# Kernel tuning notes

Hardware: AMD Instinct MI355X
Metric: run time of the kernel (lower is better)

Reference implementation:

```python
import jax, jax.numpy as jnp
import numpy as np

B, F_G, F_L, F_INT = 2, 64, 64, 32
D = H = W = 64
BN_EPS = 1e-5


def setup_inputs() -> dict:
    key = jax.random.key(0)
    ks = jax.random.split(key, 8)
    g = jax.random.normal(ks[0], (B, F_G, D, H, W), dtype=jnp.float32)
    x = jax.random.normal(ks[1], (B, F_L, D, H, W), dtype=jnp.float32)
    # Gating MLP (1x1x1 convs on pooled features == dense layers)
    w1 = jax.random.normal(ks[2], (F_INT, F_G + F_L), dtype=jnp.float32) * (1.0 / np.sqrt(F_G + F_L))
    b1 = jnp.zeros((F_INT,), dtype=jnp.float32)
    w2 = jax.random.normal(ks[3], (F_G * F_L, F_INT), dtype=jnp.float32) * (1.0 / np.sqrt(F_INT))
    b2 = jnp.zeros((F_G * F_L,), dtype=jnp.float32)
    # psi: Conv3d(F_l, 1, k=1) + BatchNorm3d(1) (inference-mode stats)
    psi_w = jax.random.normal(ks[4], (F_L,), dtype=jnp.float32) * (1.0 / np.sqrt(F_L))
    psi_b = jnp.zeros((1,), dtype=jnp.float32)
    bn_gamma = jnp.ones((1,), dtype=jnp.float32)
    bn_beta = jnp.zeros((1,), dtype=jnp.float32)
    bn_mean = jnp.zeros((1,), dtype=jnp.float32)
    bn_var = jnp.ones((1,), dtype=jnp.float32)
    return {"g": g, "x": x, "w1": w1, "b1": b1, "w2": w2, "b2": b2,
            "psi_w": psi_w, "psi_b": psi_b, "bn_gamma": bn_gamma,
            "bn_beta": bn_beta, "bn_mean": bn_mean, "bn_var": bn_var}


def reference(g, x, w1, b1, w2, b2, psi_w, psi_b, bn_gamma, bn_beta, bn_mean, bn_var):
    # Global average pool of cat([g, x]) -> [B, F_g+F_l]
    pooled = jnp.concatenate([jnp.mean(g, axis=(2, 3, 4)), jnp.mean(x, axis=(2, 3, 4))], axis=1)
    h = jax.nn.relu(pooled @ w1.T + b1)                       # [B, F_int]
    dw = jax.nn.sigmoid(h @ w2.T + b2).reshape(B, F_G, F_L)   # dynamic weights [B, F_g, F_l]
    # attended[b,l,d,h,w] = sum_g g[b,g,d,h,w] * dw[b,g,l]  (batched GEMM, no 6D blow-up)
    attended = jnp.einsum('bgdhw,bgl->bldhw', g, dw)
    # psi: 1x1x1 conv to 1 channel + BN + sigmoid
    s = jnp.einsum('bldhw,l->bdhw', attended, psi_w) + psi_b[0]
    s = (s - bn_mean[0]) * (bn_gamma[0] / jnp.sqrt(bn_var[0] + BN_EPS)) + bn_beta[0]
    return x * jax.nn.sigmoid(s)[:, None]                     # [B, F_l, D, H, W]
```

## Files before the change

### kernel.cpp

```cpp
#include <hip/hip_runtime.h>
#include <math.h>

#define SPATIAL (64*64*64)
#define SPATIAL4 (SPATIAL/4)
#define OCT4  (SPATIAL4/8)
#define NCH 64
#define BN_EPS 1e-5f

typedef float v4f __attribute__((ext_vector_type(4)));

__global__ __launch_bounds__(256, 8) void mean_kernel(const float* __restrict__ g,
                                                      const float* __restrict__ x,
                                                      float* __restrict__ partial) {
    int blk = blockIdx.x;
    int ch  = blk >> 3;
    int oct = blk & 7;
    bool isg = ch < 128;
    const float* src = isg
        ? g + (size_t)ch * SPATIAL
        : x + (size_t)(ch - 128) * SPATIAL;
    const v4f* s4 = (const v4f*)src + (size_t)oct * OCT4 + threadIdx.x;

    float acc[8] = {0.f,0.f,0.f,0.f,0.f,0.f,0.f,0.f};
    if (isg) {
        for (int it = 0; it < 4; ++it) {
            #pragma unroll
            for (int j = 0; j < 8; ++j) {
                v4f v = __builtin_nontemporal_load(s4 + j * 256);
                acc[j] += (v.x + v.y) + (v.z + v.w);
            }
            s4 += 2048;
        }
    } else {
        for (int it = 0; it < 4; ++it) {
            #pragma unroll
            for (int j = 0; j < 8; ++j) {
                v4f v = s4[j * 256];
                acc[j] += (v.x + v.y) + (v.z + v.w);
            }
            s4 += 2048;
        }
    }
    float sum = ((acc[0] + acc[1]) + (acc[2] + acc[3]))
              + ((acc[4] + acc[5]) + (acc[6] + acc[7]));

    #pragma unroll
    for (int off = 32; off > 0; off >>= 1)
        sum += __shfl_down(sum, off, 64);
    __shared__ float wsum[4];
    int lane = threadIdx.x & 63, wave = threadIdx.x >> 6;
    if (lane == 0) wsum[wave] = sum;
    __syncthreads();
    if (threadIdx.x == 0)
        partial[blk] = wsum[0] + wsum[1] + wsum[2] + wsum[3];
}

__global__ __launch_bounds__(64) void mlp_kernel(const float* __restrict__ partial,
                           const float* __restrict__ w1, const float* __restrict__ b1,
                           const float* __restrict__ w2, const float* __restrict__ b2,
                           const float* __restrict__ psi_w, const float* __restrict__ psi_b,
                           const float* __restrict__ bn_gamma, const float* __restrict__ bn_beta,
                           const float* __restrict__ bn_mean, const float* __restrict__ bn_var,
                           float* __restrict__ coef) {
    __shared__ float p[256];
    __shared__ float h[32];
    int tid = threadIdx.x;
    int blk = blockIdx.x;
    int b = blk >> 6, gc = blk & 63;

    #pragma unroll
    for (int ch = tid; ch < 256; ch += 64) {
        const float* pp = partial + 8 * ch;
        float s = ((pp[0] + pp[1]) + (pp[2] + pp[3]))
                + ((pp[4] + pp[5]) + (pp[6] + pp[7]));
        int pi = (ch < 128) ? ((ch >> 6) * 128 + (ch & 63))
                            : (((ch - 128) >> 6) * 128 + 64 + ((ch - 128) & 63));
        p[pi] = s * (1.0f / SPATIAL);
    }
    __syncthreads();
    if (tid < 32) {
        float acc = b1[tid];
        const float* wr = w1 + tid * 128;
        #pragma unroll 4
        for (int k = 0; k < 128; ++k) acc += p[b * 128 + k] * wr[k];
        h[tid] = fmaxf(acc, 0.f);
    }
    __syncthreads();
    const float4* wr = (const float4*)(w2 + (size_t)(gc * 64 + tid) * 32);
    float z = b2[gc * 64 + tid];
    #pragma unroll
    for (int j = 0; j < 8; ++j) {
        float4 wv = wr[j];
        z += h[4*j] * wv.x + h[4*j+1] * wv.y + h[4*j+2] * wv.z + h[4*j+3] * wv.w;
    }
    float sig = 1.f / (1.f + expf(-z));
    float val = sig * psi_w[tid];
    #pragma unroll
    for (int off = 32; off > 0; off >>= 1)
        val += __shfl_down(val, off, 64);
    float scale = bn_gamma[0] * rsqrtf(bn_var[0] + BN_EPS);
    if (tid == 0) coef[b * 64 + gc] = val * scale;
    if (blk == 0 && tid == 0)
        coef[128] = (psi_b[0] - bn_mean[0]) * scale + bn_beta[0];
}

__device__ __forceinline__ void fma4(v4f& a, v4f v, float c) {
    a.x += v.x * c; a.y += v.y * c; a.z += v.z * c; a.w += v.w * c;
}

__global__ __launch_bounds__(256, 8) void apply_kernel(const float* __restrict__ g,
                                                       const float* __restrict__ x,
                                                       const float* __restrict__ coef,
                                                       float* __restrict__ out) {
    int t    = threadIdx.x;
    int pos  = t & 63;
    int grp  = t >> 6;
    int blk  = blockIdx.x;
    int batch = blk >> 10;
    int base4 = (blk & 1023) * 64 + pos;
    size_t bOff = (size_t)batch * NCH * SPATIAL4;

    const v4f* g4 = (const v4f*)g;
    const v4f* x4 = (const v4f*)x;
    v4f* o4 = (v4f*)out;

    const v4f* cfv = (const v4f*)(coef + batch * NCH + grp * 16);
    const v4f* gp = g4 + bOff + (size_t)(grp * 16) * SPATIAL4 + base4;

    v4f acc0 = {0.f,0.f,0.f,0.f}, acc1 = {0.f,0.f,0.f,0.f};
    #pragma unroll
    for (int bq = 0; bq < 4; ++bq) {
        v4f cv = cfv[bq];
        v4f v0 = __builtin_nontemporal_load(gp + (size_t)(4*bq + 0) * SPATIAL4);
        v4f v1 = __builtin_nontemporal_load(gp + (size_t)(4*bq + 1) * SPATIAL4);
        v4f v2 = __builtin_nontemporal_load(gp + (size_t)(4*bq + 2) * SPATIAL4);
        v4f v3 = __builtin_nontemporal_load(gp + (size_t)(4*bq + 3) * SPATIAL4);
        fma4(acc0, v0, cv.x);
        fma4(acc1, v1, cv.y);
        fma4(acc0, v2, cv.z);
        fma4(acc1, v3, cv.w);
    }
    v4f acc = {acc0.x + acc1.x, acc0.y + acc1.y, acc0.z + acc1.z, acc0.w + acc1.w};

    __shared__ v4f red[4][64];
    if (grp != 0) red[grp][pos] = acc;
    __syncthreads();
    if (grp == 0) {
        v4f r1 = red[1][pos], r2 = red[2][pos], r3 = red[3][pos];
        float d = coef[128];
        v4f s;
        s.x = 1.f / (1.f + expf(-(acc.x + r1.x + r2.x + r3.x + d)));
        s.y = 1.f / (1.f + expf(-(acc.y + r1.y + r2.y + r3.y + d)));
        s.z = 1.f / (1.f + expf(-(acc.z + r1.z + r2.z + r3.z + d)));
        s.w = 1.f / (1.f + expf(-(acc.w + r1.w + r2.w + r3.w + d)));
        red[0][pos] = s;
    }
    __syncthreads();
    v4f s = red[0][pos];

    const v4f* xp = x4 + bOff + (size_t)(grp * 16) * SPATIAL4 + base4;
    v4f*       op = o4 + bOff + (size_t)(grp * 16) * SPATIAL4 + base4;
    #pragma unroll 4
    for (int l = 0; l < 16; ++l) {
        v4f xv = xp[(size_t)l * SPATIAL4];
        v4f ov = {xv.x * s.x, xv.y * s.y, xv.z * s.z, xv.w * s.w};
        __builtin_nontemporal_store(ov, op + (size_t)l * SPATIAL4);
    }
}

extern "C" void kernel_launch(void* const* d_in, const int* in_sizes, int n_in,
                              void* d_out, int out_size, void* d_ws, size_t ws_size,
                              hipStream_t stream) {
    const float* g        = (const float*)d_in[0];
    const float* x        = (const float*)d_in[1];
    const float* w1       = (const float*)d_in[2];
    const float* b1       = (const float*)d_in[3];
    const float* w2       = (const float*)d_in[4];
    const float* b2       = (const float*)d_in[5];
    const float* psi_w    = (const float*)d_in[6];
    const float* psi_b    = (const float*)d_in[7];
    const float* bn_gamma = (const float*)d_in[8];
    const float* bn_beta  = (const float*)d_in[9];
    const float* bn_mean  = (const float*)d_in[10];
    const float* bn_var   = (const float*)d_in[11];
    float* out = (float*)d_out;
    float* ws  = (float*)d_ws;

    float* partial = ws;
    float* coef    = ws + 2048;

    mean_kernel<<<2048, 256, 0, stream>>>(g, x, partial);
    mlp_kernel<<<128, 64, 0, stream>>>(partial, w1, b1, w2, b2, psi_w, psi_b,
                                       bn_gamma, bn_beta, bn_mean, bn_var, coef);
    apply_kernel<<<2048, 256, 0, stream>>>(g, x, coef, out);
}
```

Before: 379.5 us.

## Interleave mean-pool tiles across blocks and add a separate fold kernel

```diff
diff --git a/kernel.cpp b/kernel.cpp
--- a/kernel.cpp
+++ b/kernel.cpp
@@ -3,59 +3,60 @@
 
 #define SPATIAL (64*64*64)
 #define SPATIAL4 (SPATIAL/4)
-#define OCT4  (SPATIAL4/8)
 #define NCH 64
 #define BN_EPS 1e-5f
 
+#define NBLK   2048
+#define NTILE  65536
+#define GTILES 32768
+
 typedef float v4f __attribute__((ext_vector_type(4)));
 
-__global__ __launch_bounds__(256, 8) void mean_kernel(const float* __restrict__ g,
-                                                      const float* __restrict__ x,
-                                                      float* __restrict__ partial) {
-    int blk = blockIdx.x;
-    int ch  = blk >> 3;
-    int oct = blk & 7;
-    bool isg = ch < 128;
-    const float* src = isg
-        ? g + (size_t)ch * SPATIAL
-        : x + (size_t)(ch - 128) * SPATIAL;
-    const v4f* s4 = (const v4f*)src + (size_t)oct * OCT4 + threadIdx.x;
+__global__ __launch_bounds__(256) void mean_kernel(const float* __restrict__ g,
+                                                   const float* __restrict__ x,
+                                                   float* __restrict__ wpart) {
+    int b    = blockIdx.x;
+    int tid  = threadIdx.x;
+    int lane = tid & 63, wave = tid >> 6;
+    const v4f* g4 = (const v4f*)g;
+    const v4f* x4 = (const v4f*)x;
 
-    float acc[8] = {0.f,0.f,0.f,0.f,0.f,0.f,0.f,0.f};
-    if (isg) {
-        for (int it = 0; it < 4; ++it) {
-            #pragma unroll
-            for (int j = 0; j < 8; ++j) {
-                v4f v = __builtin_nontemporal_load(s4 + j * 256);
-                acc[j] += (v.x + v.y) + (v.z + v.w);
-            }
-            s4 += 2048;
-        }
-    } else {
-        for (int it = 0; it < 4; ++it) {
-            #pragma unroll
-            for (int j = 0; j < 8; ++j) {
-                v4f v = s4[j * 256];
-                acc[j] += (v.x + v.y) + (v.z + v.w);
-            }
-            s4 += 2048;
-        }
+    #pragma unroll 4
+    for (int k = 0; k < 32; ++k) {
+        int T = k * NBLK + b;
+        const v4f* src = (T < GTILES) ? (g4 + (size_t)T * 256)
+                                      : (x4 + (size_t)(T - GTILES) * 256);
+        v4f v = src[tid];
+        float s = (v.x + v.y) + (v.z + v.w);
+        #pragma unroll
+        for (int off = 32; off > 0; off >>= 1)
+            s += __shfl_down(s, off, 64);
+        if (lane == 0) wpart[T * 4 + wave] = s;
     }
-    float sum = ((acc[0] + acc[1]) + (acc[2] + acc[3]))
-              + ((acc[4] + acc[5]) + (acc[6] + acc[7]));
+}
 
+__global__ __launch_bounds__(256) void fold_kernel(const float* __restrict__ wpart,
+                                                   float* __restrict__ pooled) {
+    int ch  = blockIdx.x;
+    int tid = threadIdx.x;
+    const v4f* src = (const v4f*)(wpart + (size_t)ch * 1024);
+    v4f v = src[tid];
+    float s = (v.x + v.y) + (v.z + v.w);
     #pragma unroll
     for (int off = 32; off > 0; off >>= 1)
-        sum += __shfl_down(sum, off, 64);
-    __shared__ float wsum[4];
-    int lane = threadIdx.x & 63, wave = threadIdx.x >> 6;
-    if (lane == 0) wsum[wave] = sum;
+        s += __shfl_down(s, off, 64);
+    __shared__ float ws[4];
+    if ((tid & 63) == 0) ws[tid >> 6] = s;
     __syncthreads();
-    if (threadIdx.x == 0)
-        partial[blk] = wsum[0] + wsum[1] + wsum[2] + wsum[3];
+    if (tid == 0) {
+        float tot = (ws[0] + ws[1]) + (ws[2] + ws[3]);
+        int pi = (ch < 128) ? ((ch >> 6) * 128 + (ch & 63))
+                            : (((ch - 128) >> 6) * 128 + 64 + ((ch - 128) & 63));
+        pooled[pi] = tot * (1.0f / SPATIAL);
+    }
 }
 
-__global__ __launch_bounds__(64) void mlp_kernel(const float* __restrict__ partial,
+__global__ __launch_bounds__(64) void mlp_kernel(const float* __restrict__ pooled,
                            const float* __restrict__ w1, const float* __restrict__ b1,
                            const float* __restrict__ w2, const float* __restrict__ b2,
                            const float* __restrict__ psi_w, const float* __restrict__ psi_b,
@@ -69,14 +70,7 @@
     int b = blk >> 6, gc = blk & 63;
 
     #pragma unroll
-    for (int ch = tid; ch < 256; ch += 64) {
-        const float* pp = partial + 8 * ch;
-        float s = ((pp[0] + pp[1]) + (pp[2] + pp[3]))
-                + ((pp[4] + pp[5]) + (pp[6] + pp[7]));
-        int pi = (ch < 128) ? ((ch >> 6) * 128 + (ch & 63))
-                            : (((ch - 128) >> 6) * 128 + 64 + ((ch - 128) & 63));
-        p[pi] = s * (1.0f / SPATIAL);
-    }
+    for (int i = tid; i < 256; i += 64) p[i] = pooled[i];
     __syncthreads();
     if (tid < 32) {
         float acc = b1[tid];
@@ -186,11 +180,13 @@
     float* out = (float*)d_out;
     float* ws  = (float*)d_ws;
 
-    float* partial = ws;
-    float* coef    = ws + 2048;
+    float* wpart  = ws;
+    float* pooled = ws + NTILE * 4;
+    float* coef   = pooled + 256;
 
-    mean_kernel<<<2048, 256, 0, stream>>>(g, x, partial);
-    mlp_kernel<<<128, 64, 0, stream>>>(partial, w1, b1, w2, b2, psi_w, psi_b,
+    mean_kernel<<<NBLK, 256, 0, stream>>>(g, x, wpart);
+    fold_kernel<<<256, 256, 0, stream>>>(wpart, pooled);
+    mlp_kernel<<<128, 64, 0, stream>>>(pooled, w1, b1, w2, b2, psi_w, psi_b,
                                        bn_gamma, bn_beta, bn_mean, bn_var, coef);
     apply_kernel<<<2048, 256, 0, stream>>>(g, x, coef, out);
 }
```

Measured after the change: 378.1 us. About the same (-0.3%).
